# Kernel tuning notes

Hardware: AMD Instinct MI355X
Metric: run time of the kernel (lower is better)

## Reference

```python
import jax, jax.numpy as jnp
import numpy as np
from jax import lax

RHO_INT = 4            # int(rho.item()) with rho=4.0
KSIZE = 2 * RHO_INT + 1  # 9x9 GaussianBlur kernel, sigma = RHO_INT
ITER_N = 100

_SOBEL_X = jnp.array([[-1., 0., 1.], [-2., 0., 2.], [-1., 0., 1.]], jnp.float32).reshape(1, 1, 3, 3)
_SOBEL_Y = jnp.array([[-1., -2., -1.], [0., 0., 0.], [1., 2., 1.]], jnp.float32).reshape(1, 1, 3, 3)


def _gauss1d(sigma, ksize):
    # matches torchvision.transforms.GaussianBlur kernel construction
    half = (ksize - 1) / 2.0
    xs = jnp.linspace(-half, half, ksize)
    pdf = jnp.exp(-0.5 * (xs / sigma) ** 2)
    return (pdf / pdf.sum()).astype(jnp.float32)


def _conv(u, w, pad):
    # u: [B,1,H,W], w: [1,1,kh,kw]; cross-correlation like F.conv2d
    return lax.conv_general_dilated(u, w, (1, 1), pad,
                                    dimension_numbers=('NCHW', 'OIHW', 'NCHW'))


def _gauss_blur(u, k1d):
    # separable 9-tap blur with reflect padding (torchvision behavior)
    r = RHO_INT
    up = jnp.pad(u, ((0, 0), (0, 0), (r, r), (r, r)), mode='reflect')
    up = _conv(up, k1d.reshape(1, 1, KSIZE, 1), 'VALID')
    return _conv(up, k1d.reshape(1, 1, 1, KSIZE), 'VALID')


def setup_inputs() -> dict:
    key = jax.random.key(0)
    x = jax.random.uniform(key, (8, 3, 256, 256), dtype=jnp.float32)
    return {"x": x, "dt": jnp.float32(0.1), "k": jnp.float32(5.0)}


def reference(x, dt, k):
    # RGB -> luma, keep channel dim: [B,1,H,W]
    u = (0.299 * x[:, 0] + 0.587 * x[:, 1] + 0.114 * x[:, 2])[:, None]
    g1d = _gauss1d(float(RHO_INT), KSIZE)
    gauss_rho = _gauss_blur(u, g1d)  # fixed blur of initial luma, reused every iter
    k2 = k * k

    def step(u, _):
        gx = _conv(u, _SOBEL_X, 'SAME')  # zero padding=1, like F.conv2d
        gy = _conv(u, _SOBEL_Y, 'SAME')
        S11 = _gauss_blur(gx * gx, g1d) - gauss_rho
        S12 = _gauss_blur(gx * gy, g1d) - gauss_rho
        S22 = _gauss_blur(gy * gy, g1d) - gauss_rho
        tmp = jnp.sqrt((S11 - S22) ** 2 + 4.0 * S12 ** 2)
        lam1 = (S11 + S22 + tmp) * 0.5
        lam2 = (S11 + S22 - tmp) * 0.5
        c1 = jnp.exp(-(lam1 * lam1) / k2)
        c2 = jnp.exp(-(lam2 * lam2) / k2)
        return u + dt * (c1 * lam1 + c2 * lam2), None

    u, _ = lax.scan(step, u, None, length=ITER_N)
    return jnp.repeat(u, 3, axis=1)  # x had 3 channels -> repeat
```

## Files before the change

### kernel.cpp

```cpp
#include <hip/hip_runtime.h>
#include <math.h>

#define BATCH 8
#define H 256
#define W 256
#define HW (H*W)
#define KS 9
#define NSTEP 50

struct GaussW { float g[KS]; };

__device__ __forceinline__ int refl(int i, int n) {
    if (i < 0) i = -i;
    if (i >= n) i = 2*n - 2 - i;
    return i;
}

__device__ __forceinline__ float4 ld4s(const float* p) { return *(const float4*)p; }
__device__ __forceinline__ void st4s(float* p, float4 v) { *(float4*)p = v; }
__device__ __forceinline__ float4 f4mul(float a, float4 x) {
    return make_float4(a*x.x, a*x.y, a*x.z, a*x.w);
}
__device__ __forceinline__ float4 f4fma(float a, float4 x, float4 y) {
    return make_float4(fmaf(a,x.x,y.x), fmaf(a,x.y,y.y), fmaf(a,x.z,y.z), fmaf(a,x.w,y.w));
}

#if defined(__has_builtin)
#  if __has_builtin(__builtin_amdgcn_exp2f)
#    define FEXP2(x) __builtin_amdgcn_exp2f(x)
#  endif
#  if __has_builtin(__builtin_amdgcn_sqrtf)
#    define FSQRT(x) __builtin_amdgcn_sqrtf(x)
#  endif
#endif
#ifndef FEXP2
#  define FEXP2(x) exp2f(x)
#endif
#ifndef FSQRT
#  define FSQRT(x) sqrtf(x)
#endif

__device__ __forceinline__ float diffuse(float s11, float s12, float s22,
                                         float rv, float u0, float dt, float kc) {
    s11 -= rv; s12 -= rv; s22 -= rv;
    float df = s11 - s22;
    float tm = FSQRT(fmaf(df, df, 4.f*s12*s12));
    float sm = s11 + s22;
    float lam1 = 0.5f*(sm + tm);
    float lam2 = 0.5f*(sm - tm);
    float e1 = FEXP2(-(lam1*lam1)*kc);
    float e2 = FEXP2(-(lam2*lam2)*kc);
    return fmaf(dt, fmaf(e1, lam1, e2*lam2), u0);
}

template<int N>
__device__ __forceinline__ void vblur_strip(const float* __restrict__ P, float* __restrict__ V,
                                            int qoff, int r0, const GaussW gw, int stride) {
    const float* s = P + r0*stride + qoff;
    float4 w0 = ld4s(s); s += stride;
    float4 w1 = ld4s(s); s += stride;
    float4 w2 = ld4s(s); s += stride;
    float4 w3 = ld4s(s); s += stride;
    float4 w4 = ld4s(s); s += stride;
    float4 w5 = ld4s(s); s += stride;
    float4 w6 = ld4s(s); s += stride;
    float4 w7 = ld4s(s); s += stride;
    float* d = V + r0*stride + qoff;
#pragma unroll
    for (int j = 0; j < N; ++j) {
        float4 w8 = ld4s(s); s += stride;
        float4 o = f4mul(gw.g[0], w0);
        o = f4fma(gw.g[1], w1, o);
        o = f4fma(gw.g[2], w2, o);
        o = f4fma(gw.g[3], w3, o);
        o = f4fma(gw.g[4], w4, o);
        o = f4fma(gw.g[5], w5, o);
        o = f4fma(gw.g[6], w6, o);
        o = f4fma(gw.g[7], w7, o);
        o = f4fma(gw.g[8], w8, o);
        st4s(d, o); d += stride;
        w0=w1; w1=w2; w2=w3; w3=w4; w4=w5; w5=w6; w6=w7; w7=w8;
    }
}

__global__ void __launch_bounds__(512) pre_kernel(const float* __restrict__ x,
                                                  float* __restrict__ u0,
                                                  float* __restrict__ rho, GaussW gw) {
    __shared__ __align__(16) float lum[24*76];
    __shared__ __align__(16) float vb[16*72];
    const int tid = threadIdx.x;
    const int X0 = blockIdx.x*64, Y0 = blockIdx.y*16, b = blockIdx.z;
    const float* xb = x + (size_t)b*3*HW;

    if (tid < 24*18) {
        int r = tid/18, qc = tid - r*18;
        int gy = refl(Y0-4+r, H);
        int gc0 = X0-4+4*qc;
        float4 R,G,B;
        if (gc0 >= 0 && gc0+3 <= W-1) {
            const float* px = xb + gy*W + gc0;
            R = ld4s(px); G = ld4s(px+HW); B = ld4s(px+2*HW);
        } else {
            float rr[4], gg[4], bb[4];
#pragma unroll
            for (int j=0;j<4;++j){ int gc = refl(gc0+j, W);
                rr[j]=xb[gy*W+gc]; gg[j]=xb[HW+gy*W+gc]; bb[j]=xb[2*HW+gy*W+gc]; }
            R = make_float4(rr[0],rr[1],rr[2],rr[3]);
            G = make_float4(gg[0],gg[1],gg[2],gg[3]);
            B = make_float4(bb[0],bb[1],bb[2],bb[3]);
        }
        float4 L = make_float4(0.299f*R.x+0.587f*G.x+0.114f*B.x,
                               0.299f*R.y+0.587f*G.y+0.114f*B.y,
                               0.299f*R.z+0.587f*G.z+0.114f*B.z,
                               0.299f*R.w+0.587f*G.w+0.114f*B.w);
        st4s(lum + r*76 + 4*qc, L);
    }
    __syncthreads();
    if (tid < 16*18) {
        int r = tid/18, qc = tid - r*18;
        const float* s = lum + r*76 + 4*qc;
        float4 o = f4mul(gw.g[0], ld4s(s));
#pragma unroll
        for (int t = 1; t < KS; ++t) o = f4fma(gw.g[t], ld4s(s + t*76), o);
        st4s(vb + r*72 + 4*qc, o);
    }
    __syncthreads();
    if (tid < 256) {
        int r = tid>>4, c4 = tid&15;
        const float* s = vb + r*72 + 4*c4;
        float4 q0=ld4s(s), q1=ld4s(s+4), q2=ld4s(s+8);
        float f[12]={q0.x,q0.y,q0.z,q0.w,q1.x,q1.y,q1.z,q1.w,q2.x,q2.y,q2.z,q2.w};
        float o[4];
#pragma unroll
        for (int j=0;j<4;++j) {
            float a = gw.g[0]*f[j];
#pragma unroll
            for (int t=1;t<KS;++t) a = fmaf(gw.g[t], f[j+t], a);
            o[j] = a;
        }
        int gidx = b*HW + (Y0+r)*W + X0 + 4*c4;
        st4s(rho + gidx, make_float4(o[0],o[1],o[2],o[3]));
        st4s(u0 + gidx, ld4s(lum + (r+4)*76 + 4*c4 + 4));
    }
}

#define STEP_LDS_FL 28864
template<bool LAST>
__global__ void __launch_bounds__(1024, 4) step2_kernel(
        const float* __restrict__ uin, float* __restrict__ uout,
        const float* __restrict__ rho,
        const float* __restrict__ dtp, const float* __restrict__ kp,
        GaussW gw)
{
    extern __shared__ __align__(16) float lds[];
    float* su  = lds;
    float* p_  = lds + 4576;
    float* v1_ = lds + 17776;
    float* u1  = lds;
    float* q_  = lds + 4576;
    float* w_  = lds + 17776;

    const int tid = threadIdx.x;
    const int X0 = blockIdx.x*64, Y0 = blockIdx.y*32, b = blockIdx.z;
    const float* ub = uin + b*HW;
    const float* rb = rho + b*HW;
    const float dt = *dtp;
    const float kk = *kp;
    const float kc = 1.4426950408889634f / (kk*kk);

    if (tid < 572) {
        int r = tid/11, cp = tid - r*11;
        int gy = Y0-10+r, gc = X0-12+8*cp;
        float4 a = make_float4(0,0,0,0), c = make_float4(0,0,0,0);
        if (gy>=0 && gy<H) {
            if (gc>=0 && gc<=W-4)     a = ld4s(ub + gy*W + gc);
            if (gc+4>=0 && gc+4<=W-4) c = ld4s(ub + gy*W + gc+4);
        }
        float* d = su + r*88 + 8*cp;
        st4s(d, a); st4s(d+4, c);
    }
    __syncthreads();

    if (tid < 550) {
        int pr = tid/11, cp = tid - pr*11;
        int sr = refl(Y0-9+pr, H) - (Y0-10);
        int qA = 8*cp-4; if (qA<0) qA=0;
        int qB = 8*cp;
        int qD = 8*cp+8; if (qD>84) qD=84;
        const float* rm = su + (sr-1)*88;
        const float* rc = su + sr*88;
        const float* rp = su + (sr+1)*88;
        float4 Am=ld4s(rm+qA), Bm=ld4s(rm+qB), Cm=ld4s(rm+qB+4), Dm=ld4s(rm+qD);
        float4 Ac=ld4s(rc+qA), Bc=ld4s(rc+qB), Cc=ld4s(rc+qB+4), Dc=ld4s(rc+qD);
        float4 Ap=ld4s(rp+qA), Bp=ld4s(rp+qB), Cp=ld4s(rp+qB+4), Dp=ld4s(rp+qD);
        float fm[10]={Am.w,Bm.x,Bm.y,Bm.z,Bm.w,Cm.x,Cm.y,Cm.z,Cm.w,Dm.x};
        float fc[10]={Ac.w,Bc.x,Bc.y,Bc.z,Bc.w,Cc.x,Cc.y,Cc.z,Cc.w,Dc.x};
        float fp[10]={Ap.w,Bp.x,Bp.y,Bp.z,Bp.w,Cp.x,Cp.y,Cp.z,Cp.w,Dp.x};
        float o11[8],o12[8],o22[8];
#pragma unroll
        for (int j=0;j<8;++j) {
            float gx = (fm[j+2]-fm[j]) + 2.f*(fc[j+2]-fc[j]) + (fp[j+2]-fp[j]);
            float gy = (fp[j]-fm[j]) + 2.f*(fp[j+1]-fm[j+1]) + (fp[j+2]-fm[j+2]);
            o11[j]=gx*gx; o12[j]=gx*gy; o22[j]=gy*gy;
        }
        int o = pr*88 + 8*cp;
        st4s(p_+o,        make_float4(o11[0],o11[1],o11[2],o11[3]));
        st4s(p_+o+4,      make_float4(o11[4],o11[5],o11[6],o11[7]));
        st4s(p_+4400+o,   make_float4(o12[0],o12[1],o12[2],o12[3]));
        st4s(p_+4400+o+4, make_float4(o12[4],o12[5],o12[6],o12[7]));
        st4s(p_+8800+o,   make_float4(o22[0],o22[1],o22[2],o22[3]));
        st4s(p_+8800+o+4, make_float4(o22[4],o22[5],o22[6],o22[7]));
    }
    __syncthreads();

    if (tid < 462) {
        int cg = tid % 22; int t = tid / 22; int strip = t % 7; int plane = t / 7;
        vblur_strip<6>(p_ + plane*4400, v1_ + plane*3696, 4*cg, strip*6, gw, 88);
    }
    __syncthreads();

    if (X0 == 0) {
        for (int i = tid; i < 3*42*9; i += 1024) {
            int j = i%9+1; int t = i/9; int r = t%42; int pl = t/42;
            float* V = v1_ + pl*3696 + r*88;
            V[12-j] = V[12+j];
        }
    } else if (X0 == W-64) {
        for (int i = tid; i < 3*42*9; i += 1024) {
            int j = i%9+1; int t = i/9; int r = t%42; int pl = t/42;
            float* V = v1_ + pl*3696 + r*88;
            V[75+j] = V[75-j];
        }
    }
    __syncthreads();

    if (tid < 420) {
        int r = tid/10, cp = tid - r*10;
        int uy = Y0-5+r;
        int c0 = X0-8+8*cp;
        float acc[3][8];
#pragma unroll
        for (int pl=0; pl<3; ++pl) {
            const float* Vp = v1_ + pl*3696 + r*88 + 8*cp;
            float4 q0=ld4s(Vp), q1=ld4s(Vp+4), q2=ld4s(Vp+8), q3=ld4s(Vp+12);
            float f[16]={q0.x,q0.y,q0.z,q0.w,q1.x,q1.y,q1.z,q1.w,
                         q2.x,q2.y,q2.z,q2.w,q3.x,q3.y,q3.z,q3.w};
#pragma unroll
            for (int j=0;j<8;++j) {
                float s = gw.g[0]*f[j];
#pragma unroll
                for (int t=1;t<KS;++t) s = fmaf(gw.g[t], f[j+t], s);
                acc[pl][j] = s;
            }
        }
        bool rowin = (uy>=0 && uy<H);
        bool in0 = rowin && c0>=0   && c0<=W-4;
        bool in1 = rowin && c0+4>=0 && c0+4<=W-4;
        float4 rv0=make_float4(0,0,0,0), rv1=rv0, uq0=rv0, uq1=rv0;
        if (in0) { rv0 = ld4s(rb+uy*W+c0);   uq0 = ld4s(ub+uy*W+c0); }
        if (in1) { rv1 = ld4s(rb+uy*W+c0+4); uq1 = ld4s(ub+uy*W+c0+4); }
        float rva[8]={rv0.x,rv0.y,rv0.z,rv0.w,rv1.x,rv1.y,rv1.z,rv1.w};
        float uqa[8]={uq0.x,uq0.y,uq0.z,uq0.w,uq1.x,uq1.y,uq1.z,uq1.w};
        float res[8];
#pragma unroll
        for (int j=0;j<8;++j)
            res[j] = diffuse(acc[0][j],acc[1][j],acc[2][j],rva[j],uqa[j],dt,kc);
        float* d = u1 + r*80 + 8*cp;
        st4s(d,   in0 ? make_float4(res[0],res[1],res[2],res[3]) : make_float4(0,0,0,0));
        st4s(d+4, in1 ? make_float4(res[4],res[5],res[6],res[7]) : make_float4(0,0,0,0));
    }
    __syncthreads();

    if (tid < 400) {
        int pr = tid/10, cp = tid - pr*10;
        int ur = refl(Y0-4+pr, H) - (Y0-5);
        int qA = 8*cp-4; if (qA<0) qA=0;
        int qB = 8*cp;
        int qD = 8*cp+8; if (qD>76) qD=76;
        const float* rm = u1 + (ur-1)*80;
        const float* rc = u1 + ur*80;
        const float* rp = u1 + (ur+1)*80;
        float4 Am=ld4s(rm+qA), Bm=ld4s(rm+qB), Cm=ld4s(rm+qB+4), Dm=ld4s(rm+qD);
        float4 Ac=ld4s(rc+qA), Bc=ld4s(rc+qB), Cc=ld4s(rc+qB+4), Dc=ld4s(rc+qD);
        float4 Ap=ld4s(rp+qA), Bp=ld4s(rp+qB), Cp=ld4s(rp+qB+4), Dp=ld4s(rp+qD);
        float fm[10]={Am.w,Bm.x,Bm.y,Bm.z,Bm.w,Cm.x,Cm.y,Cm.z,Cm.w,Dm.x};
        float fc[10]={Ac.w,Bc.x,Bc.y,Bc.z,Bc.w,Cc.x,Cc.y,Cc.z,Cc.w,Dc.x};
        float fp[10]={Ap.w,Bp.x,Bp.y,Bp.z,Bp.w,Cp.x,Cp.y,Cp.z,Cp.w,Dp.x};
        float o11[8],o12[8],o22[8];
#pragma unroll
        for (int j=0;j<8;++j) {
            float gx = (fm[j+2]-fm[j]) + 2.f*(fc[j+2]-fc[j]) + (fp[j+2]-fp[j]);
            float gy = (fp[j]-fm[j]) + 2.f*(fp[j+1]-fm[j+1]) + (fp[j+2]-fm[j+2]);
            o11[j]=gx*gx; o12[j]=gx*gy; o22[j]=gy*gy;
        }
        int o = pr*80 + 8*cp;
        st4s(q_+o,        make_float4(o11[0],o11[1],o11[2],o11[3]));
        st4s(q_+o+4,      make_float4(o11[4],o11[5],o11[6],o11[7]));
        st4s(q_+3200+o,   make_float4(o12[0],o12[1],o12[2],o12[3]));
        st4s(q_+3200+o+4, make_float4(o12[4],o12[5],o12[6],o12[7]));
        st4s(q_+6400+o,   make_float4(o22[0],o22[1],o22[2],o22[3]));
        st4s(q_+6400+o+4, make_float4(o22[4],o22[5],o22[6],o22[7]));
    }
    __syncthreads();

    if (tid < 240) {
        int cg = tid % 20; int t = tid/20; int strip = t % 4; int pl = t / 4;
        vblur_strip<8>(q_ + pl*3200, w_ + pl*2560, 4*cg, strip*8, gw, 80);
    }
    __syncthreads();

    if (X0 == 0) {
        if (tid < 384) { int j = tid%4+1; int t = tid/4; int r = t%32; int pl = t/32;
            float* V = w_ + pl*2560 + r*80; V[8-j] = V[8+j]; }
    } else if (X0 == W-64) {
        if (tid < 384) { int j = tid%4+1; int t = tid/4; int r = t%32; int pl = t/32;
            float* V = w_ + pl*2560 + r*80; V[71+j] = V[71-j]; }
    }
    __syncthreads();

    if (tid < 512) {
        int r = tid>>4, c4 = tid&15;
        float acc[3][4];
#pragma unroll
        for (int pl=0; pl<3; ++pl) {
            const float* Vp = w_ + pl*2560 + r*80 + 4*c4 + 4;
            float4 q0=ld4s(Vp), q1=ld4s(Vp+4), q2=ld4s(Vp+8);
            float f[12]={q0.x,q0.y,q0.z,q0.w,q1.x,q1.y,q1.z,q1.w,q2.x,q2.y,q2.z,q2.w};
#pragma unroll
            for (int j=0;j<4;++j) {
                float s = gw.g[0]*f[j];
#pragma unroll
                for (int t=1;t<KS;++t) s = fmaf(gw.g[t], f[j+t], s);
                acc[pl][j] = s;
            }
        }
        int gidx = (Y0+r)*W + X0 + 4*c4;
        float4 rv = ld4s(rb + gidx);
        float4 uq = ld4s(u1 + (r+5)*80 + 4*c4 + 8);
        float rva[4]={rv.x,rv.y,rv.z,rv.w};
        float uqa[4]={uq.x,uq.y,uq.z,uq.w};
        float o[4];
#pragma unroll
        for (int j=0;j<4;++j)
            o[j] = diffuse(acc[0][j],acc[1][j],acc[2][j],rva[j],uqa[j],dt,kc);
        float4 ov = make_float4(o[0],o[1],o[2],o[3]);
        if (LAST) {
            float* ob = uout + (size_t)b*3*HW + gidx;
            st4s(ob, ov); st4s(ob+HW, ov); st4s(ob+2*HW, ov);
        } else {
            st4s(uout + b*HW + gidx, ov);
        }
    }
}

extern "C" void kernel_launch(void* const* d_in, const int* in_sizes, int n_in,
                              void* d_out, int out_size, void* d_ws, size_t ws_size,
                              hipStream_t stream) {
    const float* x   = (const float*)d_in[0];
    const float* dtp = (const float*)d_in[1];
    const float* kp  = (const float*)d_in[2];
    float* out = (float*)d_out;

    float* u_a = (float*)d_ws;
    float* u_b = u_a + BATCH*HW;
    float* rho = u_b + BATCH*HW;

    GaussW gw;
    {
        double s = 0.0, wd[KS];
        for (int i = 0; i < KS; ++i) {
            double xd = (double)i - 4.0;
            wd[i] = exp(-0.5 * (xd/4.0) * (xd/4.0));
            s += wd[i];
        }
        for (int i = 0; i < KS; ++i) gw.g[i] = (float)(wd[i] / s);
    }

    const int dyn_lds = STEP_LDS_FL * 4;
    (void)hipFuncSetAttribute((const void*)step2_kernel<false>,
                              hipFuncAttributeMaxDynamicSharedMemorySize, dyn_lds);
    (void)hipFuncSetAttribute((const void*)step2_kernel<true>,
                              hipFuncAttributeMaxDynamicSharedMemorySize, dyn_lds);

    dim3 gpre(W/64, H/16, BATCH), bpre(512);
    pre_kernel<<<gpre, bpre, 0, stream>>>(x, u_a, rho, gw);

    dim3 gs(W/64, H/32, BATCH), bs(1024);
    float* cur = u_a;
    float* nxt = u_b;
    for (int it = 0; it < NSTEP-1; ++it) {
        step2_kernel<false><<<gs, bs, dyn_lds, stream>>>(cur, nxt, rho, dtp, kp, gw);
        float* t = cur; cur = nxt; nxt = t;
    }
    step2_kernel<true><<<gs, bs, dyn_lds, stream>>>(cur, out, rho, dtp, kp, gw);
}
```

Baseline: 626.2 us.

## Load Sobel inputs from global, fuse edge reflection into blur, shrink second-step tiles

The first Sobel stage now reads the input image directly from global memory with bounds checks, which removes the staging of u into shared memory and one barrier. The reflected edge columns of the vertical blur are now computed directly from the source planes in the same pass as the blur, instead of being copied in a separate pass after another barrier. The second sub-step trims its halo width from 80 to 72 columns, which cuts work and shared memory so that more blocks may fit per CU. The cost is more global loads per thread and branch divergence in the merged loops.

```diff
diff --git a/kernel.cpp b/kernel.cpp
--- a/kernel.cpp
+++ b/kernel.cpp
@@ -144,7 +144,7 @@
     }
 }
 
-#define STEP_LDS_FL 28864
+#define STEP_LDS_FL 24288
 template<bool LAST>
 __global__ void __launch_bounds__(1024, 4) step2_kernel(
         const float* __restrict__ uin, float* __restrict__ uout,
@@ -153,12 +153,11 @@
         GaussW gw)
 {
     extern __shared__ __align__(16) float lds[];
-    float* su  = lds;
-    float* p_  = lds + 4576;
-    float* v1_ = lds + 17776;
-    float* u1  = lds;
-    float* q_  = lds + 4576;
-    float* w_  = lds + 17776;
+    float* p_ = lds;
+    float* v_ = lds + 13200;
+    float* u1 = lds;
+    float* q_ = lds + 3360;
+    float* w_ = lds + 13200;
 
     const int tid = threadIdx.x;
     const int X0 = blockIdx.x*64, Y0 = blockIdx.y*32, b = blockIdx.z;
@@ -167,32 +166,26 @@
     const float dt = *dtp;
     const float kk = *kp;
     const float kc = 1.4426950408889634f / (kk*kk);
-
-    if (tid < 572) {
-        int r = tid/11, cp = tid - r*11;
-        int gy = Y0-10+r, gc = X0-12+8*cp;
-        float4 a = make_float4(0,0,0,0), c = make_float4(0,0,0,0);
-        if (gy>=0 && gy<H) {
-            if (gc>=0 && gc<=W-4)     a = ld4s(ub + gy*W + gc);
-            if (gc+4>=0 && gc+4<=W-4) c = ld4s(ub + gy*W + gc+4);
-        }
-        float* d = su + r*88 + 8*cp;
-        st4s(d, a); st4s(d+4, c);
-    }
-    __syncthreads();
+    const bool eL = (X0 == 0), eR = (X0 == W-64);
+    const float4 f4z = make_float4(0.f,0.f,0.f,0.f);
 
     if (tid < 550) {
-        int pr = tid/11, cp = tid - pr*11;
-        int sr = refl(Y0-9+pr, H) - (Y0-10);
-        int qA = 8*cp-4; if (qA<0) qA=0;
-        int qB = 8*cp;
-        int qD = 8*cp+8; if (qD>84) qD=84;
-        const float* rm = su + (sr-1)*88;
-        const float* rc = su + sr*88;
-        const float* rp = su + (sr+1)*88;
-        float4 Am=ld4s(rm+qA), Bm=ld4s(rm+qB), Cm=ld4s(rm+qB+4), Dm=ld4s(rm+qD);
-        float4 Ac=ld4s(rc+qA), Bc=ld4s(rc+qB), Cc=ld4s(rc+qB+4), Dc=ld4s(rc+qD);
-        float4 Ap=ld4s(rp+qA), Bp=ld4s(rp+qB), Cp=ld4s(rp+qB+4), Dp=ld4s(rp+qD);
+        int pr = tid / 11, cg = tid - pr*11;
+        int c0 = X0 - 12 + 8*cg;
+        int p0 = refl(Y0 - 9 + pr, H);
+        const float* rc = ub + p0*W;
+        const float* rm = rc - W;
+        const float* rp = rc + W;
+        bool mok = (p0 > 0), pok = (p0 < H-1);
+        int cA = c0-4, cB = c0, cC = c0+4, cD = c0+8;
+        bool aok = (cA >= 0 && cA <= W-4), bok = (cB >= 0 && cB <= W-4);
+        bool cok = (cC >= 0 && cC <= W-4), dok = (cD >= 0 && cD <= W-4);
+        float4 Am = (mok&&aok)?ld4s(rm+cA):f4z, Bm = (mok&&bok)?ld4s(rm+cB):f4z;
+        float4 Cm = (mok&&cok)?ld4s(rm+cC):f4z, Dm = (mok&&dok)?ld4s(rm+cD):f4z;
+        float4 Ac = aok?ld4s(rc+cA):f4z,        Bc = bok?ld4s(rc+cB):f4z;
+        float4 Cc = cok?ld4s(rc+cC):f4z,        Dc = dok?ld4s(rc+cD):f4z;
+        float4 Ap = (pok&&aok)?ld4s(rp+cA):f4z, Bp = (pok&&bok)?ld4s(rp+cB):f4z;
+        float4 Cp = (pok&&cok)?ld4s(rp+cC):f4z, Dp = (pok&&dok)?ld4s(rp+cD):f4z;
         float fm[10]={Am.w,Bm.x,Bm.y,Bm.z,Bm.w,Cm.x,Cm.y,Cm.z,Cm.w,Dm.x};
         float fc[10]={Ac.w,Bc.x,Bc.y,Bc.z,Bc.w,Cc.x,Cc.y,Cc.z,Cc.w,Dc.x};
         float fp[10]={Ap.w,Bp.x,Bp.y,Bp.z,Bp.w,Cp.x,Cp.y,Cp.z,Cp.w,Dp.x};
@@ -203,7 +196,7 @@
             float gy = (fp[j]-fm[j]) + 2.f*(fp[j+1]-fm[j+1]) + (fp[j+2]-fm[j+2]);
             o11[j]=gx*gx; o12[j]=gx*gy; o22[j]=gy*gy;
         }
-        int o = pr*88 + 8*cp;
+        int o = pr*88 + 8*cg;
         st4s(p_+o,        make_float4(o11[0],o11[1],o11[2],o11[3]));
         st4s(p_+o+4,      make_float4(o11[4],o11[5],o11[6],o11[7]));
         st4s(p_+4400+o,   make_float4(o12[0],o12[1],o12[2],o12[3]));
@@ -213,23 +206,25 @@
     }
     __syncthreads();
 
-    if (tid < 462) {
-        int cg = tid % 22; int t = tid / 22; int strip = t % 7; int plane = t / 7;
-        vblur_strip<6>(p_ + plane*4400, v1_ + plane*3696, 4*cg, strip*6, gw, 88);
-    }
-    __syncthreads();
-
-    if (X0 == 0) {
-        for (int i = tid; i < 3*42*9; i += 1024) {
-            int j = i%9+1; int t = i/9; int r = t%42; int pl = t/42;
-            float* V = v1_ + pl*3696 + r*88;
-            V[12-j] = V[12+j];
-        }
-    } else if (X0 == W-64) {
-        for (int i = tid; i < 3*42*9; i += 1024) {
-            int j = i%9+1; int t = i/9; int r = t%42; int pl = t/42;
-            float* V = v1_ + pl*3696 + r*88;
-            V[75+j] = V[75-j];
+    {
+        int nTot = 462 + ((eL || eR) ? 1134 : 0);
+        for (int i = tid; i < nTot; i += 1024) {
+            if (i < 462) {
+                int cg = i % 22; int t = i / 22; int strip = t % 7; int pl = t / 7;
+                if (eL && cg < 3) continue;
+                if (eR && cg > 18) continue;
+                vblur_strip<6>(p_ + pl*4400, v_ + pl*3696, 4*cg, strip*6, gw, 88);
+            } else {
+                int g = i - 462;
+                int j = 1 + (g % 9); int t = g / 9; int rr = t % 42; int pl = t / 42;
+                const float* P = p_ + pl*4400;
+                int dst = eL ? (12 - j) : (75 + j);
+                int src = eL ? (12 + j) : (75 - j);
+                float a = 0.f;
+#pragma unroll
+                for (int t2 = 0; t2 < KS; ++t2) a = fmaf(gw.g[t2], P[(rr+t2)*88 + src], a);
+                (v_ + pl*3696)[rr*88 + dst] = a;
+            }
         }
     }
     __syncthreads();
@@ -241,7 +236,7 @@
         float acc[3][8];
 #pragma unroll
         for (int pl=0; pl<3; ++pl) {
-            const float* Vp = v1_ + pl*3696 + r*88 + 8*cp;
+            const float* Vp = v_ + pl*3696 + r*88 + 8*cp;
             float4 q0=ld4s(Vp), q1=ld4s(Vp+4), q2=ld4s(Vp+8), q3=ld4s(Vp+12);
             float f[16]={q0.x,q0.y,q0.z,q0.w,q1.x,q1.y,q1.z,q1.w,
                          q2.x,q2.y,q2.z,q2.w,q3.x,q3.y,q3.z,q3.w};
@@ -256,7 +251,7 @@
         bool rowin = (uy>=0 && uy<H);
         bool in0 = rowin && c0>=0   && c0<=W-4;
         bool in1 = rowin && c0+4>=0 && c0+4<=W-4;
-        float4 rv0=make_float4(0,0,0,0), rv1=rv0, uq0=rv0, uq1=rv0;
+        float4 rv0=f4z, rv1=f4z, uq0=f4z, uq1=f4z;
         if (in0) { rv0 = ld4s(rb+uy*W+c0);   uq0 = ld4s(ub+uy*W+c0); }
         if (in1) { rv1 = ld4s(rb+uy*W+c0+4); uq1 = ld4s(ub+uy*W+c0+4); }
         float rva[8]={rv0.x,rv0.y,rv0.z,rv0.w,rv1.x,rv1.y,rv1.z,rv1.w};
@@ -266,23 +261,20 @@
         for (int j=0;j<8;++j)
             res[j] = diffuse(acc[0][j],acc[1][j],acc[2][j],rva[j],uqa[j],dt,kc);
         float* d = u1 + r*80 + 8*cp;
-        st4s(d,   in0 ? make_float4(res[0],res[1],res[2],res[3]) : make_float4(0,0,0,0));
-        st4s(d+4, in1 ? make_float4(res[4],res[5],res[6],res[7]) : make_float4(0,0,0,0));
-    }
-    __syncthreads();
-
-    if (tid < 400) {
-        int pr = tid/10, cp = tid - pr*10;
-        int ur = refl(Y0-4+pr, H) - (Y0-5);
-        int qA = 8*cp-4; if (qA<0) qA=0;
-        int qB = 8*cp;
-        int qD = 8*cp+8; if (qD>76) qD=76;
-        const float* rm = u1 + (ur-1)*80;
-        const float* rc = u1 + ur*80;
-        const float* rp = u1 + (ur+1)*80;
-        float4 Am=ld4s(rm+qA), Bm=ld4s(rm+qB), Cm=ld4s(rm+qB+4), Dm=ld4s(rm+qD);
-        float4 Ac=ld4s(rc+qA), Bc=ld4s(rc+qB), Cc=ld4s(rc+qB+4), Dc=ld4s(rc+qD);
-        float4 Ap=ld4s(rp+qA), Bp=ld4s(rp+qB), Cp=ld4s(rp+qB+4), Dp=ld4s(rp+qD);
+        st4s(d,   in0 ? make_float4(res[0],res[1],res[2],res[3]) : f4z);
+        st4s(d+4, in1 ? make_float4(res[4],res[5],res[6],res[7]) : f4z);
+    }
+    __syncthreads();
+
+    if (tid < 360) {
+        int pr = tid / 9, cg = tid - pr*9;
+        int sr = refl(Y0-4+pr, H) - (Y0-5);
+        const float* rm = u1 + (sr-1)*80 + 8*cg;
+        const float* rc = rm + 80;
+        const float* rp = rc + 80;
+        float4 Am=ld4s(rm), Bm=ld4s(rm+4), Cm=ld4s(rm+8), Dm=ld4s(rm+12);
+        float4 Ac=ld4s(rc), Bc=ld4s(rc+4), Cc=ld4s(rc+8), Dc=ld4s(rc+12);
+        float4 Ap=ld4s(rp), Bp=ld4s(rp+4), Cp=ld4s(rp+8), Dp=ld4s(rp+12);
         float fm[10]={Am.w,Bm.x,Bm.y,Bm.z,Bm.w,Cm.x,Cm.y,Cm.z,Cm.w,Dm.x};
         float fc[10]={Ac.w,Bc.x,Bc.y,Bc.z,Bc.w,Cc.x,Cc.y,Cc.z,Cc.w,Dc.x};
         float fp[10]={Ap.w,Bp.x,Bp.y,Bp.z,Bp.w,Cp.x,Cp.y,Cp.z,Cp.w,Dp.x};
@@ -293,28 +285,36 @@
             float gy = (fp[j]-fm[j]) + 2.f*(fp[j+1]-fm[j+1]) + (fp[j+2]-fm[j+2]);
             o11[j]=gx*gx; o12[j]=gx*gy; o22[j]=gy*gy;
         }
-        int o = pr*80 + 8*cp;
+        int o = pr*72 + 8*cg;
         st4s(q_+o,        make_float4(o11[0],o11[1],o11[2],o11[3]));
         st4s(q_+o+4,      make_float4(o11[4],o11[5],o11[6],o11[7]));
-        st4s(q_+3200+o,   make_float4(o12[0],o12[1],o12[2],o12[3]));
-        st4s(q_+3200+o+4, make_float4(o12[4],o12[5],o12[6],o12[7]));
-        st4s(q_+6400+o,   make_float4(o22[0],o22[1],o22[2],o22[3]));
-        st4s(q_+6400+o+4, make_float4(o22[4],o22[5],o22[6],o22[7]));
-    }
-    __syncthreads();
-
-    if (tid < 240) {
-        int cg = tid % 20; int t = tid/20; int strip = t % 4; int pl = t / 4;
-        vblur_strip<8>(q_ + pl*3200, w_ + pl*2560, 4*cg, strip*8, gw, 80);
-    }
-    __syncthreads();
-
-    if (X0 == 0) {
-        if (tid < 384) { int j = tid%4+1; int t = tid/4; int r = t%32; int pl = t/32;
-            float* V = w_ + pl*2560 + r*80; V[8-j] = V[8+j]; }
-    } else if (X0 == W-64) {
-        if (tid < 384) { int j = tid%4+1; int t = tid/4; int r = t%32; int pl = t/32;
-            float* V = w_ + pl*2560 + r*80; V[71+j] = V[71-j]; }
+        st4s(q_+2880+o,   make_float4(o12[0],o12[1],o12[2],o12[3]));
+        st4s(q_+2880+o+4, make_float4(o12[4],o12[5],o12[6],o12[7]));
+        st4s(q_+5760+o,   make_float4(o22[0],o22[1],o22[2],o22[3]));
+        st4s(q_+5760+o+4, make_float4(o22[4],o22[5],o22[6],o22[7]));
+    }
+    __syncthreads();
+
+    {
+        int n2 = 216 + ((eL || eR) ? 384 : 0);
+        if (tid < n2) {
+            if (tid < 216) {
+                int cg = tid % 18; int t = tid/18; int strip = t % 4; int pl = t/4;
+                bool skip = (eL && cg == 0) || (eR && cg == 17);
+                if (!skip)
+                    vblur_strip<8>(q_ + pl*2880, w_ + pl*2304, 4*cg, strip*8, gw, 72);
+            } else {
+                int g = tid - 216;
+                int j = 1 + (g & 3); int t = g >> 2; int rr = t % 32; int pl = t / 32;
+                const float* Q = q_ + pl*2880;
+                int dst = eL ? (4-j) : (67+j);
+                int src = eL ? (4+j) : (67-j);
+                float a = 0.f;
+#pragma unroll
+                for (int t2 = 0; t2 < KS; ++t2) a = fmaf(gw.g[t2], Q[(rr+t2)*72 + src], a);
+                (w_ + pl*2304)[rr*72 + dst] = a;
+            }
+        }
     }
     __syncthreads();
 
@@ -323,7 +323,7 @@
         float acc[3][4];
 #pragma unroll
         for (int pl=0; pl<3; ++pl) {
-            const float* Vp = w_ + pl*2560 + r*80 + 4*c4 + 4;
+            const float* Vp = w_ + pl*2304 + r*72 + 4*c4;
             float4 q0=ld4s(Vp), q1=ld4s(Vp+4), q2=ld4s(Vp+8);
             float f[12]={q0.x,q0.y,q0.z,q0.w,q1.x,q1.y,q1.z,q1.w,q2.x,q2.y,q2.z,q2.w};
 #pragma unroll
```

New measurement: 592.5 us. 5.4% less time.
